# Performance work log

Measured on AMD Instinct MI355X. Metric: run time of the kernel, lower is better.

Reference implementation:

```python
import jax, jax.numpy as jnp
import numpy as np

L, H, DK = 4, 8, 64
NEG = -1e9
PAD = -9999.0


def _ln(z, g, b, eps=1e-6):
    # LayerNormalization: uses unbiased std (torch default) and divides by (std + eps)
    m = jnp.mean(z, axis=-1, keepdims=True)
    s = jnp.std(z, axis=-1, keepdims=True, ddof=1)
    return g * (z - m) / (s + eps) + b


def _mha(q_in, kv_in, w, bw, pw, pb, lnp, mask):
    B, Sq, D = q_in.shape
    q = (q_in @ w[0] + bw[0]).reshape(B, Sq, H, DK).transpose(0, 2, 1, 3)
    k = (kv_in @ w[1] + bw[1]).reshape(B, -1, H, DK).transpose(0, 2, 1, 3)
    v = (kv_in @ w[2] + bw[2]).reshape(B, -1, H, DK).transpose(0, 2, 1, 3)
    scores = jnp.einsum('bhqd,bhkd->bhqk', q, k) * (1.0 / np.sqrt(DK))
    if mask is not None:
        scores = jnp.where(mask[:, None, :, :], NEG, scores)
    attn = jax.nn.softmax(scores, axis=-1)
    ctx = jnp.einsum('bhqk,bhkd->bhqd', attn, v).transpose(0, 2, 1, 3).reshape(B, Sq, H * DK)
    return _ln(q_in + ctx @ pw + pb, lnp[0], lnp[1])


def _ffn(x, w1, b1, w2, b2, lnp):
    # kernel-1 conv1d == pointwise linear; w1:[d_ff,d_model], w2:[d_model,d_ff]
    h = jax.nn.relu(jnp.einsum('bsd,fd->bsf', x, w1) + b1)
    o = jnp.einsum('bsf,df->bsd', h, w2) + b2
    return _ln(x + o, lnp[0], lnp[1])


def _forward(enc_inputs, dec_inputs, emb_w, emb_b, pos_table,
             e_qkv_w, e_qkv_b, e_pw, e_pb, e_ln1, e_w1, e_b1, e_w2, e_b2, e_ln2,
             ds_qkv_w, ds_qkv_b, ds_pw, ds_pb, d_ln1,
             dc_qkv_w, dc_qkv_b, dc_pw, dc_pb, d_ln2,
             d_w1, d_b1, d_w2, d_b2, d_ln3):
    B, Se, F = enc_inputs.shape
    Sd = dec_inputs.shape[1]
    # ConvEmbeddingLayer: kernel-1 conv producing (d_model - n_features) channels, concat with raw inputs
    enc = jnp.concatenate([enc_inputs, jnp.einsum('bsf,of->bso', enc_inputs, emb_w) + emb_b], axis=-1)
    dec = jnp.concatenate([dec_inputs, jnp.einsum('bsf,of->bso', dec_inputs, emb_w) + emb_b], axis=-1)
    # PosEncoding with full lengths -> rows 1..S of the padded table
    enc = enc + pos_table[1:Se + 1]
    dec = dec + pos_table[1:Sd + 1]
    # masks per get_attn_pad_mask / get_attn_subsequent_mask
    enc_pad = jnp.sum(enc_inputs, axis=-1) <= PAD  # [B,Se]
    dec_pad = jnp.sum(dec_inputs, axis=-1) <= PAD  # [B,Sd]
    enc_mask = jnp.broadcast_to(enc_pad[:, None, :], (B, Se, Se))
    causal = jnp.triu(jnp.ones((Sd, Sd), dtype=bool), 1)
    dec_self_mask = jnp.broadcast_to(dec_pad[:, None, :], (B, Sd, Sd)) | causal
    cross_mask = jnp.broadcast_to(enc_pad[:, None, :], (B, Sd, Se))
    for i in range(L):
        enc = _mha(enc, enc, e_qkv_w[i], e_qkv_b[i], e_pw[i], e_pb[i], e_ln1[i], enc_mask)
        enc = _ffn(enc, e_w1[i], e_b1[i], e_w2[i], e_b2[i], e_ln2[i])
    for i in range(L):
        dec = _mha(dec, dec, ds_qkv_w[i], ds_qkv_b[i], ds_pw[i], ds_pb[i], d_ln1[i], dec_self_mask)
        dec = _mha(dec, enc, dc_qkv_w[i], dc_qkv_b[i], dc_pw[i], dc_pb[i], d_ln2[i], cross_mask)
        dec = _ffn(dec, d_w1[i], d_b1[i], d_w2[i], d_b2[i], d_ln3[i])
    return dec


def setup_inputs() -> dict:
    B, Se, Sd, F, Dm, Dff = 8, 512, 512, 32, 512, 2048
    key = jax.random.key(0)
    ks = iter(jax.random.split(key, 32))
    s = 0.02

    def n(shape, sc=s):
        return jax.random.normal(next(ks), shape, jnp.float32) * sc

    # sinusoidal PosEncoding table with leading pad row
    pos = np.arange(Se, dtype=np.float64)[:, None]
    j = np.arange(Dm)[None, :]
    ang = pos / np.power(10000.0, 2.0 * (j // 2) / Dm)
    ang[:, 0::2] = np.sin(ang[:, 0::2])
    ang[:, 1::2] = np.cos(ang[:, 1::2])
    pos_table = jnp.asarray(np.concatenate([np.zeros((1, Dm)), ang]).astype(np.float32))

    ln = jnp.broadcast_to(jnp.stack([jnp.ones(Dm), jnp.zeros(Dm)]), (L, 2, Dm)).astype(jnp.float32) + 0.0
    return {
        'enc_inputs': jax.random.normal(next(ks), (B, Se, F), jnp.float32),
        'dec_inputs': jax.random.normal(next(ks), (B, Sd, F), jnp.float32),
        'emb_w': n((Dm - F, F)), 'emb_b': jnp.zeros(Dm - F, jnp.float32),
        'pos_table': pos_table,
        'e_qkv_w': n((L, 3, Dm, H * DK)), 'e_qkv_b': jnp.zeros((L, 3, H * DK), jnp.float32),
        'e_pw': n((L, H * DK, Dm)), 'e_pb': jnp.zeros((L, Dm), jnp.float32), 'e_ln1': ln,
        'e_w1': n((L, Dff, Dm)), 'e_b1': jnp.zeros((L, Dff), jnp.float32),
        'e_w2': n((L, Dm, Dff)), 'e_b2': jnp.zeros((L, Dm), jnp.float32), 'e_ln2': ln,
        'ds_qkv_w': n((L, 3, Dm, H * DK)), 'ds_qkv_b': jnp.zeros((L, 3, H * DK), jnp.float32),
        'ds_pw': n((L, H * DK, Dm)), 'ds_pb': jnp.zeros((L, Dm), jnp.float32), 'd_ln1': ln,
        'dc_qkv_w': n((L, 3, Dm, H * DK)), 'dc_qkv_b': jnp.zeros((L, 3, H * DK), jnp.float32),
        'dc_pw': n((L, H * DK, Dm)), 'dc_pb': jnp.zeros((L, Dm), jnp.float32), 'd_ln2': ln,
        'd_w1': n((L, Dff, Dm)), 'd_b1': jnp.zeros((L, Dff), jnp.float32),
        'd_w2': n((L, Dm, Dff)), 'd_b2': jnp.zeros((L, Dm), jnp.float32), 'd_ln3': ln,
    }


def reference(enc_inputs, dec_inputs, emb_w, emb_b, pos_table,
              e_qkv_w, e_qkv_b, e_pw, e_pb, e_ln1, e_w1, e_b1, e_w2, e_b2, e_ln2,
              ds_qkv_w, ds_qkv_b, ds_pw, ds_pb, d_ln1,
              dc_qkv_w, dc_qkv_b, dc_pw, dc_pb, d_ln2,
              d_w1, d_b1, d_w2, d_b2, d_ln3):
    return _forward(enc_inputs, dec_inputs, emb_w, emb_b, pos_table,
                    e_qkv_w, e_qkv_b, e_pw, e_pb, e_ln1, e_w1, e_b1, e_w2, e_b2, e_ln2,
                    ds_qkv_w, ds_qkv_b, ds_pw, ds_pb, d_ln1,
                    dc_qkv_w, dc_qkv_b, dc_pw, dc_pb, d_ln2,
                    d_w1, d_b1, d_w2, d_b2, d_ln3)
```

## Files before the change

kernel.cpp:

```cpp
#include <hip/hip_runtime.h>
#include <cstdint>
#include <cstddef>

typedef unsigned short u16;
typedef __bf16 bf16x8 __attribute__((ext_vector_type(8)));
typedef float f32x4 __attribute__((ext_vector_type(4)));

constexpr int Bz = 8, Sq = 512, Hh = 8, DKd = 64, Dm = 512, Dff = 2048, NL = 4;
constexpr int TOK = Bz * Sq;
constexpr size_t MAT = (size_t)512 * 512;
constexpr size_t EL  = (size_t)TOK * Dm;
constexpr size_t WFT = (size_t)Dff * Dm;

__device__ __forceinline__ float bf2f(u16 u) {
  union { uint32_t i; float f; } v; v.i = (uint32_t)u << 16; return v.f;
}
__device__ __forceinline__ u16 f2bf(float f) {
  union { float f; uint32_t i; } v; v.f = f;
  uint32_t i = v.i;
  i += 0x7fffu + ((i >> 16) & 1u);
  return (u16)(i >> 16);
}

__device__ __forceinline__ void gload16(const u16* g, u16* l) {
  __builtin_amdgcn_global_load_lds(
      (const __attribute__((address_space(1))) unsigned int*)g,
      (__attribute__((address_space(3))) unsigned int*)l, 16, 0, 0);
}

template<int BM, int BN>
__global__ __launch_bounds__(256)
void gemm_tile(const u16* __restrict__ A, const u16* __restrict__ Bt,
               const float* __restrict__ bias, u16* __restrict__ C,
               int K, int lda, long long sA, int ldb, long long sB,
               int ldc, long long sC, int cmode, int relu, int colofs,
               const u16* A2, int xsplit)
{
  constexpr int HM = BM / 2, HN = BN / 2, MI = HM / 16, NI = HN / 16;
  __shared__ __align__(16) u16 As[BM * 64];
  __shared__ __align__(16) u16 Bs[BN * 64];
  const int bz = blockIdx.z;
  const u16* Abase = A;
  int colbase;
  if (A2 && (int)blockIdx.x >= xsplit) {
    Abase = A2;
    colbase = 512 + ((int)blockIdx.x - xsplit) * BN;
  } else {
    colbase = colofs + (int)blockIdx.x * BN;
  }
  const u16* Ab = Abase + (size_t)bz * (size_t)sA + (size_t)(blockIdx.y * BM) * lda;
  const u16* Bb = Bt + (size_t)bz * (size_t)sB + (size_t)colbase * ldb;
  const int tid  = threadIdx.x;
  const int lane = tid & 63;
  const int wid  = tid >> 6;
  const int l15  = lane & 15;
  const int quad = lane >> 4;
  const int wm   = wid >> 1, wn = wid & 1;

  f32x4 acc[MI][NI] = {};

  for (int k0 = 0; k0 < K; k0 += 64) {
#pragma unroll
    for (int i = 0; i < BM / 32; ++i) {
      const int s = tid + i * 256;
      const int row = s >> 3, c = (s & 7) ^ (row & 7);
      gload16(Ab + (size_t)row * lda + k0 + c * 8, As + s * 8);
    }
#pragma unroll
    for (int i = 0; i < BN / 32; ++i) {
      const int s = tid + i * 256;
      const int row = s >> 3, c = (s & 7) ^ (row & 7);
      gload16(Bb + (size_t)row * ldb + k0 + c * 8, Bs + s * 8);
    }
    __syncthreads();
#pragma unroll
    for (int kk = 0; kk < 2; ++kk) {
      bf16x8 af[MI], bfr[NI];
#pragma unroll
      for (int mi = 0; mi < MI; ++mi) {
        const int ra = wm * HM + mi * 16 + l15;
        af[mi] = *(const bf16x8*)(As + ra * 64 + (((kk * 4 + quad) ^ (ra & 7))) * 8);
      }
#pragma unroll
      for (int ni = 0; ni < NI; ++ni) {
        const int rb = wn * HN + ni * 16 + l15;
        bfr[ni] = *(const bf16x8*)(Bs + rb * 64 + (((kk * 4 + quad) ^ (rb & 7))) * 8);
      }
#pragma unroll
      for (int mi = 0; mi < MI; ++mi)
#pragma unroll
        for (int ni = 0; ni < NI; ++ni)
          acc[mi][ni] = __builtin_amdgcn_mfma_f32_16x16x32_bf16(af[mi], bfr[ni], acc[mi][ni], 0, 0, 0);
    }
    __syncthreads();
  }

  const int rblk = blockIdx.y * BM + wm * HM + quad * 4;
#pragma unroll
  for (int ni = 0; ni < NI; ++ni) {
    const int colx = colbase + wn * HN + ni * 16 + l15;
    const float bv = bias ? bias[colx] : 0.f;
#pragma unroll
    for (int mi = 0; mi < MI; ++mi) {
#pragma unroll
      for (int r = 0; r < 4; ++r) {
        float v = acc[mi][ni][r] + bv;
        if (relu) v = fmaxf(v, 0.f);
        const int grow = rblk + mi * 16 + r;
        size_t off;
        if (cmode == 0) {
          off = (size_t)bz * (size_t)sC + (size_t)grow * ldc + colx;
        } else {
          const int sec = colx >> 9, n = colx & 511, h = n >> 6, d = n & 63;
          const int b = grow >> 9, s = grow & 511;
          if (sec == 0) v *= 0.125f;
          if (sec < 2) off = (size_t)sec * EL + (size_t)b * 262144 + (size_t)h * 32768 + (size_t)s * 64 + d;
          else         off = 2 * EL + (size_t)b * 262144 + (size_t)h * 32768 + (size_t)d * 512 + s;
        }
        C[off] = f2bf(v);
      }
    }
  }
}

__global__ __launch_bounds__(256)
void flash_attn(const u16* __restrict__ q, const u16* __restrict__ k,
                const u16* __restrict__ v, const unsigned char* __restrict__ pad,
                u16* __restrict__ ctx, int mtype)
{
  __shared__ __align__(16) u16 KVs[8192];
  __shared__ __align__(16) u16 Pw[4][2048];
  const int bh = blockIdx.y, b = bh >> 3, h = bh & 7;
  const int qt = blockIdx.x;
  const int tid = threadIdx.x, lane = tid & 63, wid = tid >> 6;
  const int l15 = lane & 15, quad = lane >> 4;
  const size_t bho = (size_t)bh * 32768;
  const int qrow = qt * 64 + wid * 16 + l15;
  const int qcd  = qt * 64 + wid * 16 + quad * 4;

  unsigned char* Ps = (unsigned char*)&Pw[0][0];
  if (tid < 128) ((uchar4*)Ps)[tid] = ((const uchar4*)(pad + b * 512))[tid];

  bf16x8 aq0 = *(const bf16x8*)(q + bho + (size_t)qrow * 64 + quad * 8);
  bf16x8 aq1 = *(const bf16x8*)(q + bho + (size_t)qrow * 64 + 32 + quad * 8);

  f32x4 S[32];
#pragma unroll
  for (int kc = 0; kc < 4; ++kc) {
    __syncthreads();
#pragma unroll
    for (int i = 0; i < 4; ++i) {
      const int s = tid + i * 256;
      const int row = s >> 3, c = (s & 7) ^ (row & 7);
      gload16(k + bho + (size_t)(kc * 128 + row) * 64 + c * 8, KVs + s * 8);
    }
    __syncthreads();
#pragma unroll
    for (int t = 0; t < 8; ++t) {
      const int sw = l15 & 7;
      bf16x8 b0 = *(const bf16x8*)(KVs + (t * 16 + l15) * 64 + (quad ^ sw) * 8);
      bf16x8 b1 = *(const bf16x8*)(KVs + (t * 16 + l15) * 64 + ((4 + quad) ^ sw) * 8);
      f32x4 z = {0.f, 0.f, 0.f, 0.f};
      z = __builtin_amdgcn_mfma_f32_16x16x32_bf16(aq0, b0, z, 0, 0, 0);
      S[kc * 8 + t] = __builtin_amdgcn_mfma_f32_16x16x32_bf16(aq1, b1, z, 0, 0, 0);
    }
  }

  unsigned pm = 0u;
#pragma unroll
  for (int t = 0; t < 32; ++t) pm |= (unsigned)(Ps[t * 16 + l15] != 0) << t;

  float inv[4];
#pragma unroll
  for (int r = 0; r < 4; ++r) {
    const int qg = qcd + r;
    float mx = -3.0e38f;
#pragma unroll
    for (int t = 0; t < 32; ++t) {
      const int col = t * 16 + l15;
      const bool m = ((pm >> t) & 1u) || (mtype == 1 && col > qg);
      const float val = m ? -1e9f : S[t][r];
      S[t][r] = val;
      mx = fmaxf(mx, val);
    }
#pragma unroll
    for (int o = 8; o > 0; o >>= 1) mx = fmaxf(mx, __shfl_xor(mx, o));
    float sm = 0.f;
#pragma unroll
    for (int t = 0; t < 32; ++t) { const float e = __expf(S[t][r] - mx); S[t][r] = e; sm += e; }
#pragma unroll
    for (int o = 8; o > 0; o >>= 1) sm += __shfl_xor(sm, o);
    inv[r] = 1.f / sm;
  }

  f32x4 O[4] = {};
  u16* myP = &Pw[wid][0];
#pragma unroll
  for (int kc = 0; kc < 4; ++kc) {
    __syncthreads();
#pragma unroll
    for (int i = 0; i < 4; ++i) {
      const int s = tid + i * 256;
      const int row = s >> 4, c = (s & 15) ^ (row & 15);
      gload16(v + bho + (size_t)row * 512 + kc * 128 + c * 8, KVs + s * 8);
    }
#pragma unroll
    for (int t = 0; t < 8; ++t)
#pragma unroll
      for (int r = 0; r < 4; ++r) {
        const int rowq = quad * 4 + r;
        const int c = 2 * t + (l15 >> 3);
        myP[rowq * 128 + (c ^ rowq) * 8 + (l15 & 7)] = f2bf(S[kc * 8 + t][r] * inv[r]);
      }
    __syncthreads();
#pragma unroll
    for (int kk = 0; kk < 4; ++kk) {
      bf16x8 ap = *(const bf16x8*)(myP + l15 * 128 + ((kk * 4 + quad) ^ l15) * 8);
#pragma unroll
      for (int ni = 0; ni < 4; ++ni) {
        bf16x8 bv = *(const bf16x8*)(KVs + (ni * 16 + l15) * 128 + ((kk * 4 + quad) ^ l15) * 8);
        O[ni] = __builtin_amdgcn_mfma_f32_16x16x32_bf16(ap, bv, O[ni], 0, 0, 0);
      }
    }
  }

  const int token = b * 512 + qcd;
#pragma unroll
  for (int ni = 0; ni < 4; ++ni)
#pragma unroll
    for (int r = 0; r < 4; ++r)
      ctx[(size_t)(token + r) * 512 + h * 64 + ni * 16 + l15] = f2bf(O[ni][r]);
}

__global__ __launch_bounds__(256)
void transpose_all(const float* __restrict__ s0, const float* __restrict__ s1,
                   const float* __restrict__ s2, const float* __restrict__ s3,
                   const float* __restrict__ s4, const float* __restrict__ s5,
                   u16* __restrict__ out)
{
  __shared__ float tile[32][33];
  const int z = blockIdx.z;
  const float* src; int zi;
  if      (z < 12) { src = s0; zi = z; }
  else if (z < 24) { src = s1; zi = z - 12; }
  else if (z < 36) { src = s2; zi = z - 24; }
  else if (z < 40) { src = s3; zi = z - 36; }
  else if (z < 44) { src = s4; zi = z - 40; }
  else             { src = s5; zi = z - 44; }
  const float* in = src + (size_t)zi * MAT;
  u16* o = out + (size_t)z * MAT;
  int x = blockIdx.x * 32 + threadIdx.x;
  int y = blockIdx.y * 32 + threadIdx.y;
#pragma unroll
  for (int i = 0; i < 32; i += 8)
    tile[threadIdx.y + i][threadIdx.x] = in[(size_t)(y + i) * 512 + x];
  __syncthreads();
  x = blockIdx.y * 32 + threadIdx.x;
  y = blockIdx.x * 32 + threadIdx.y;
#pragma unroll
  for (int i = 0; i < 32; i += 8)
    o[(size_t)(y + i) * 512 + x] = f2bf(tile[threadIdx.x][threadIdx.y + i]);
}

__global__ __launch_bounds__(256)
void convert4(const float* __restrict__ a, const float* __restrict__ b,
              const float* __restrict__ c, const float* __restrict__ d,
              u16* __restrict__ out, int n)
{
  const float* srcs[4] = { a, b, c, d };
  const float* src = srcs[blockIdx.y];
  u16* dst = out + (size_t)blockIdx.y * n;
  int i = (blockIdx.x * 256 + threadIdx.x) * 4;
  if (i < n) {
    float4 v = *(const float4*)(src + i);
    ushort4 u = { f2bf(v.x), f2bf(v.y), f2bf(v.z), f2bf(v.w) };
    *(ushort4*)(dst + i) = u;
  }
}

__global__ __launch_bounds__(256)
void embed_k(const float* __restrict__ x, const float* __restrict__ ew,
             const float* __restrict__ eb, const float* __restrict__ pos,
             u16* __restrict__ out, unsigned char* __restrict__ padv)
{
  const int rs = blockIdx.x;
  const int s  = rs & 511;
  __shared__ float xr[32];
  const int t = threadIdx.x;
  if (t < 32) xr[t] = x[(size_t)rs * 32 + t];
  __syncthreads();
  if (t == 0) {
    float sacc = 0.f;
#pragma unroll
    for (int f = 0; f < 32; ++f) sacc += xr[f];
    padv[rs] = (sacc <= -9999.f) ? 1 : 0;
  }
#pragma unroll
  for (int rep = 0; rep < 2; ++rep) {
    const int c = t + rep * 256;
    float v;
    if (c < 32) {
      v = xr[c];
    } else {
      const float* w = ew + (size_t)(c - 32) * 32;
      float acc = eb[c - 32];
#pragma unroll
      for (int f = 0; f < 32; ++f) acc += xr[f] * w[f];
      v = acc;
    }
    v += pos[(size_t)(s + 1) * 512 + c];
    out[(size_t)rs * 512 + c] = f2bf(v);
  }
}

__global__ __launch_bounds__(256)
void add_ln(const u16* __restrict__ x, const u16* __restrict__ y,
            const float* __restrict__ g, const float* __restrict__ bb,
            u16* __restrict__ out)
{
  const int row  = blockIdx.x * 4 + (threadIdx.x >> 6);
  const int lane = threadIdx.x & 63;
  const int c0 = lane * 8;
  const size_t base = (size_t)row * Dm + c0;

  uint4 xr = *(const uint4*)(x + base);
  uint4 yr = *(const uint4*)(y + base);
  const u16* xh = (const u16*)&xr;
  const u16* yh = (const u16*)&yr;
  float z[8];
  float s = 0.f;
#pragma unroll
  for (int j = 0; j < 8; ++j) { z[j] = bf2f(xh[j]) + bf2f(yh[j]); s += z[j]; }
#pragma unroll
  for (int off = 32; off > 0; off >>= 1) s += __shfl_xor(s, off);
  const float mean = s * (1.f / 512.f);
  float ss = 0.f;
#pragma unroll
  for (int j = 0; j < 8; ++j) { z[j] -= mean; ss += z[j] * z[j]; }
#pragma unroll
  for (int off = 32; off > 0; off >>= 1) ss += __shfl_xor(ss, off);
  const float stdv = sqrtf(ss * (1.f / 511.f));
  const float inv = 1.f / (stdv + 1e-6f);

  float4 g0 = *(const float4*)(g + c0),  g1 = *(const float4*)(g + c0 + 4);
  float4 b0 = *(const float4*)(bb + c0), b1 = *(const float4*)(bb + c0 + 4);
  float gv[8] = { g0.x, g0.y, g0.z, g0.w, g1.x, g1.y, g1.z, g1.w };
  float bv[8] = { b0.x, b0.y, b0.z, b0.w, b1.x, b1.y, b1.z, b1.w };
  uint4 ow;
  u16* oh = (u16*)&ow;
#pragma unroll
  for (int j = 0; j < 8; ++j) oh[j] = f2bf(gv[j] * z[j] * inv + bv[j]);
  *(uint4*)(out + base) = ow;
}

__global__ __launch_bounds__(256)
void store_f32(const u16* __restrict__ in, float* __restrict__ out, int n)
{
  int i = (blockIdx.x * 256 + threadIdx.x) * 8;
  if (i < n) {
    uint4 raw = *(const uint4*)(in + i);
    const u16* h = (const u16*)&raw;
    float4 o0 = { bf2f(h[0]), bf2f(h[1]), bf2f(h[2]), bf2f(h[3]) };
    float4 o1 = { bf2f(h[4]), bf2f(h[5]), bf2f(h[6]), bf2f(h[7]) };
    *(float4*)(out + i) = o0;
    *(float4*)(out + i + 4) = o1;
  }
}

extern "C" void kernel_launch(void* const* d_in, const int* in_sizes, int n_in,
                              void* d_out, int out_size, void* d_ws, size_t ws_size,
                              hipStream_t stream)
{
  (void)in_sizes; (void)n_in; (void)out_size;
  const float* enc_in   = (const float*)d_in[0];
  const float* dec_in   = (const float*)d_in[1];
  const float* emb_w    = (const float*)d_in[2];
  const float* emb_b    = (const float*)d_in[3];
  const float* pos      = (const float*)d_in[4];
  const float* e_qkv_w  = (const float*)d_in[5];
  const float* e_qkv_b  = (const float*)d_in[6];
  const float* e_pw     = (const float*)d_in[7];
  const float* e_pb     = (const float*)d_in[8];
  const float* e_ln1    = (const float*)d_in[9];
  const float* e_w1     = (const float*)d_in[10];
  const float* e_b1     = (const float*)d_in[11];
  const float* e_w2     = (const float*)d_in[12];
  const float* e_b2     = (const float*)d_in[13];
  const float* e_ln2    = (const float*)d_in[14];
  const float* ds_qkv_w = (const float*)d_in[15];
  const float* ds_qkv_b = (const float*)d_in[16];
  const float* ds_pw    = (const float*)d_in[17];
  const float* ds_pb    = (const float*)d_in[18];
  const float* d_ln1    = (const float*)d_in[19];
  const float* dc_qkv_w = (const float*)d_in[20];
  const float* dc_qkv_b = (const float*)d_in[21];
  const float* dc_pw    = (const float*)d_in[22];
  const float* dc_pb    = (const float*)d_in[23];
  const float* d_ln2    = (const float*)d_in[24];
  const float* d_w1     = (const float*)d_in[25];
  const float* d_b1     = (const float*)d_in[26];
  const float* d_w2     = (const float*)d_in[27];
  const float* d_b2     = (const float*)d_in[28];
  const float* d_ln3    = (const float*)d_in[29];

  u16* ws  = (u16*)d_ws;
  u16* enc = ws;
  u16* dec = ws + EL;
  u16* qb  = ws + 2 * EL;
  u16* kb  = ws + 3 * EL;
  u16* vT  = ws + 4 * EL;
  u16* ctx = ws + 5 * EL;
  u16* t1  = ws + 6 * EL;
  u16* hff = ws + 7 * EL;
  u16* wT  = ws + 15 * EL;
  unsigned char* padE = (unsigned char*)(ws + 21 * EL);
  unsigned char* padD = padE + TOK;
  u16* wfAll = ws + 22 * EL;
  if (ws_size < 30 * EL * 2 + 2 * TOK) return;

  transpose_all<<<dim3(16, 16, 48), dim3(32, 8), 0, stream>>>(
      e_qkv_w, ds_qkv_w, dc_qkv_w, e_pw, ds_pw, dc_pw, wT);
  convert4<<<dim3(4096, 4), 256, 0, stream>>>(e_w1, e_w2, d_w1, d_w2, wfAll, (int)(4 * WFT));
  embed_k<<<TOK, 256, 0, stream>>>(enc_in, emb_w, emb_b, pos, enc, padE);
  embed_k<<<TOK, 256, 0, stream>>>(dec_in, emb_w, emb_b, pos, dec, padD);

  auto attention = [&](const u16* qsrc, const u16* kvsrc, const u16* wq3, const float* b3,
                       const u16* pwT, const float* pb, const float* ln,
                       const unsigned char* pad, int mtype, u16* x) {
    if (qsrc == kvsrc) {
      gemm_tile<64, 128><<<dim3(12, 64, 1), 256, 0, stream>>>(
          qsrc, wq3, b3, qb, 512, 512, 0, 512, 0, 0, 0, 4, 0, 0, nullptr, 0);
    } else {
      gemm_tile<64, 128><<<dim3(12, 64, 1), 256, 0, stream>>>(
          qsrc, wq3, b3, qb, 512, 512, 0, 512, 0, 0, 0, 4, 0, 0, kvsrc, 4);
    }
    flash_attn<<<dim3(8, 64), 256, 0, stream>>>(qb, kb, vT, pad, ctx, mtype);
    gemm_tile<64, 64><<<dim3(8, 64, 1), 256, 0, stream>>>(
        ctx, pwT, pb, t1, 512, 512, 0, 512, 0, 512, 0, 0, 0, 0, nullptr, 0);
    add_ln<<<TOK / 4, 256, 0, stream>>>(x, t1, ln, ln + 512, x);
  };

  auto ffn = [&](u16* x, const u16* w1b, const float* b1, const u16* w2b,
                 const float* b2, const float* ln) {
    gemm_tile<128, 128><<<dim3(16, 32, 1), 256, 0, stream>>>(
        x, w1b, b1, hff, 512, 512, 0, 512, 0, 2048, 0, 0, 1, 0, nullptr, 0);
    gemm_tile<64, 64><<<dim3(8, 64, 1), 256, 0, stream>>>(
        hff, w2b, b2, t1, 2048, 2048, 0, 2048, 0, 512, 0, 0, 0, 0, nullptr, 0);
    add_ln<<<TOK / 4, 256, 0, stream>>>(x, t1, ln, ln + 512, x);
  };

  for (int i = 0; i < NL; ++i) {
    attention(enc, enc, wT + (size_t)(i * 3) * MAT, e_qkv_b + i * 3 * 512,
              wT + (size_t)(36 + i) * MAT, e_pb + i * 512, e_ln1 + i * 1024, padE, 0, enc);
    ffn(enc, wfAll + (size_t)i * WFT, e_b1 + i * Dff,
        wfAll + 4 * WFT + (size_t)i * WFT, e_b2 + i * Dm, e_ln2 + i * 1024);
  }

  for (int i = 0; i < NL; ++i) {
    attention(dec, dec, wT + (size_t)(12 + i * 3) * MAT, ds_qkv_b + i * 3 * 512,
              wT + (size_t)(40 + i) * MAT, ds_pb + i * 512, d_ln1 + i * 1024, padD, 1, dec);
    attention(dec, enc, wT + (size_t)(24 + i * 3) * MAT, dc_qkv_b + i * 3 * 512,
              wT + (size_t)(44 + i) * MAT, dc_pb + i * 512, d_ln2 + i * 1024, padE, 2, dec);
    ffn(dec, wfAll + 8 * WFT + (size_t)i * WFT, d_b1 + i * Dff,
        wfAll + 12 * WFT + (size_t)i * WFT, d_b2 + i * Dm, d_ln3 + i * 1024);
  }

  store_f32<<<(int)(EL / 8 / 256), 256, 0, stream>>>(dec, (float*)d_out, (int)EL);
}
```

Baseline: 1.301 ms.

## Deepen GEMM K-tile to 128, shrink FFN1 tile, merge prep kernels and fuse final store

The GEMM template gains a BK parameter and every GEMM now stages 128-wide K slices in LDS, with an extended XOR swizzle. This halves the number of barrier-separated iterations at the cost of larger LDS use per block. The FFN up-projection moves from 128x128 to 64x128 tiles to launch more blocks. Separately, the weight transpose and convert kernels are merged into one launch, the two embedding launches into one, and the final fp32 store is folded into the last layernorm, which removes launches and one pass over the output.

```diff
diff --git a/kernel.cpp b/kernel.cpp
--- a/kernel.cpp
+++ b/kernel.cpp
@@ -28,7 +28,7 @@
       (__attribute__((address_space(3))) unsigned int*)l, 16, 0, 0);
 }
 
-template<int BM, int BN>
+template<int BM, int BN, int BK>
 __global__ __launch_bounds__(256)
 void gemm_tile(const u16* __restrict__ A, const u16* __restrict__ Bt,
                const float* __restrict__ bias, u16* __restrict__ C,
@@ -37,8 +37,9 @@
                const u16* A2, int xsplit)
 {
   constexpr int HM = BM / 2, HN = BN / 2, MI = HM / 16, NI = HN / 16;
-  __shared__ __align__(16) u16 As[BM * 64];
-  __shared__ __align__(16) u16 Bs[BN * 64];
+  constexpr int CPR = BK / 8;
+  __shared__ __align__(16) u16 As[BM * BK];
+  __shared__ __align__(16) u16 Bs[BN * BK];
   const int bz = blockIdx.z;
   const u16* Abase = A;
   int colbase;
@@ -59,32 +60,38 @@
 
   f32x4 acc[MI][NI] = {};
 
-  for (int k0 = 0; k0 < K; k0 += 64) {
-#pragma unroll
-    for (int i = 0; i < BM / 32; ++i) {
+  for (int k0 = 0; k0 < K; k0 += BK) {
+#pragma unroll
+    for (int i = 0; i < (BM * CPR) / 256; ++i) {
       const int s = tid + i * 256;
-      const int row = s >> 3, c = (s & 7) ^ (row & 7);
+      const int row = s / CPR, cl = s % CPR;
+      const int c = (cl & 8) | ((cl ^ row) & 7);
       gload16(Ab + (size_t)row * lda + k0 + c * 8, As + s * 8);
     }
 #pragma unroll
-    for (int i = 0; i < BN / 32; ++i) {
+    for (int i = 0; i < (BN * CPR) / 256; ++i) {
       const int s = tid + i * 256;
-      const int row = s >> 3, c = (s & 7) ^ (row & 7);
+      const int row = s / CPR, cl = s % CPR;
+      const int c = (cl & 8) | ((cl ^ row) & 7);
       gload16(Bb + (size_t)row * ldb + k0 + c * 8, Bs + s * 8);
     }
     __syncthreads();
 #pragma unroll
-    for (int kk = 0; kk < 2; ++kk) {
+    for (int kk = 0; kk < BK / 32; ++kk) {
       bf16x8 af[MI], bfr[NI];
 #pragma unroll
       for (int mi = 0; mi < MI; ++mi) {
         const int ra = wm * HM + mi * 16 + l15;
-        af[mi] = *(const bf16x8*)(As + ra * 64 + (((kk * 4 + quad) ^ (ra & 7))) * 8);
+        const int ch = kk * 4 + quad;
+        const int sw = (ch & 8) | ((ch ^ ra) & 7);
+        af[mi] = *(const bf16x8*)(As + ra * BK + sw * 8);
       }
 #pragma unroll
       for (int ni = 0; ni < NI; ++ni) {
         const int rb = wn * HN + ni * 16 + l15;
-        bfr[ni] = *(const bf16x8*)(Bs + rb * 64 + (((kk * 4 + quad) ^ (rb & 7))) * 8);
+        const int ch = kk * 4 + quad;
+        const int sw = (ch & 8) | ((ch ^ rb) & 7);
+        bfr[ni] = *(const bf16x8*)(Bs + rb * BK + sw * 8);
       }
 #pragma unroll
       for (int mi = 0; mi < MI; ++mi)
@@ -233,45 +240,45 @@
 }
 
 __global__ __launch_bounds__(256)
-void transpose_all(const float* __restrict__ s0, const float* __restrict__ s1,
-                   const float* __restrict__ s2, const float* __restrict__ s3,
-                   const float* __restrict__ s4, const float* __restrict__ s5,
-                   u16* __restrict__ out)
+void prep_weights(const float* __restrict__ s0, const float* __restrict__ s1,
+                  const float* __restrict__ s2, const float* __restrict__ s3,
+                  const float* __restrict__ s4, const float* __restrict__ s5,
+                  u16* __restrict__ outT,
+                  const float* __restrict__ c0, const float* __restrict__ c1,
+                  const float* __restrict__ c2, const float* __restrict__ c3,
+                  u16* __restrict__ outC)
 {
   __shared__ float tile[32][33];
   const int z = blockIdx.z;
-  const float* src; int zi;
-  if      (z < 12) { src = s0; zi = z; }
-  else if (z < 24) { src = s1; zi = z - 12; }
-  else if (z < 36) { src = s2; zi = z - 24; }
-  else if (z < 40) { src = s3; zi = z - 36; }
-  else if (z < 44) { src = s4; zi = z - 40; }
-  else             { src = s5; zi = z - 44; }
-  const float* in = src + (size_t)zi * MAT;
-  u16* o = out + (size_t)z * MAT;
-  int x = blockIdx.x * 32 + threadIdx.x;
-  int y = blockIdx.y * 32 + threadIdx.y;
-#pragma unroll
-  for (int i = 0; i < 32; i += 8)
-    tile[threadIdx.y + i][threadIdx.x] = in[(size_t)(y + i) * 512 + x];
-  __syncthreads();
-  x = blockIdx.y * 32 + threadIdx.x;
-  y = blockIdx.x * 32 + threadIdx.y;
-#pragma unroll
-  for (int i = 0; i < 32; i += 8)
-    o[(size_t)(y + i) * 512 + x] = f2bf(tile[threadIdx.x][threadIdx.y + i]);
-}
-
-__global__ __launch_bounds__(256)
-void convert4(const float* __restrict__ a, const float* __restrict__ b,
-              const float* __restrict__ c, const float* __restrict__ d,
-              u16* __restrict__ out, int n)
-{
-  const float* srcs[4] = { a, b, c, d };
-  const float* src = srcs[blockIdx.y];
-  u16* dst = out + (size_t)blockIdx.y * n;
-  int i = (blockIdx.x * 256 + threadIdx.x) * 4;
-  if (i < n) {
+  if (z < 48) {
+    const float* src; int zi;
+    if      (z < 12) { src = s0; zi = z; }
+    else if (z < 24) { src = s1; zi = z - 12; }
+    else if (z < 36) { src = s2; zi = z - 24; }
+    else if (z < 40) { src = s3; zi = z - 36; }
+    else if (z < 44) { src = s4; zi = z - 40; }
+    else             { src = s5; zi = z - 44; }
+    const float* in = src + (size_t)zi * MAT;
+    u16* o = outT + (size_t)z * MAT;
+    int x = blockIdx.x * 32 + threadIdx.x;
+    int y = blockIdx.y * 32 + threadIdx.y;
+#pragma unroll
+    for (int i = 0; i < 32; i += 8)
+      tile[threadIdx.y + i][threadIdx.x] = in[(size_t)(y + i) * 512 + x];
+    __syncthreads();
+    x = blockIdx.y * 32 + threadIdx.x;
+    y = blockIdx.x * 32 + threadIdx.y;
+#pragma unroll
+    for (int i = 0; i < 32; i += 8)
+      o[(size_t)(y + i) * 512 + x] = f2bf(tile[threadIdx.x][threadIdx.y + i]);
+  } else {
+    const int tid = threadIdx.y * 32 + threadIdx.x;
+    const int L = (z - 48) * 256 + blockIdx.y * 16 + blockIdx.x;
+    const int tens = L >> 12, bx = L & 4095;
+    const float* srcs[4] = { c0, c1, c2, c3 };
+    const float* src = srcs[tens];
+    u16* dst = outC + (size_t)tens * (4 * WFT);
+    const int i = (bx * 256 + tid) * 4;
     float4 v = *(const float4*)(src + i);
     ushort4 u = { f2bf(v.x), f2bf(v.y), f2bf(v.z), f2bf(v.w) };
     *(ushort4*)(dst + i) = u;
@@ -279,10 +286,15 @@
 }
 
 __global__ __launch_bounds__(256)
-void embed_k(const float* __restrict__ x, const float* __restrict__ ew,
-             const float* __restrict__ eb, const float* __restrict__ pos,
-             u16* __restrict__ out, unsigned char* __restrict__ padv)
-{
+void embed2(const float* __restrict__ xe, const float* __restrict__ xd,
+            const float* __restrict__ ew, const float* __restrict__ eb,
+            const float* __restrict__ pos,
+            u16* __restrict__ oute, u16* __restrict__ outd,
+            unsigned char* __restrict__ pe, unsigned char* __restrict__ pd)
+{
+  const float* x = blockIdx.y ? xd : xe;
+  u16* out = blockIdx.y ? outd : oute;
+  unsigned char* padv = blockIdx.y ? pd : pe;
   const int rs = blockIdx.x;
   const int s  = rs & 511;
   __shared__ float xr[32];
@@ -316,7 +328,7 @@
 __global__ __launch_bounds__(256)
 void add_ln(const u16* __restrict__ x, const u16* __restrict__ y,
             const float* __restrict__ g, const float* __restrict__ bb,
-            u16* __restrict__ out)
+            u16* __restrict__ out, float* __restrict__ out32)
 {
   const int row  = blockIdx.x * 4 + (threadIdx.x >> 6);
   const int lane = threadIdx.x & 63;
@@ -346,24 +358,20 @@
   float4 b0 = *(const float4*)(bb + c0), b1 = *(const float4*)(bb + c0 + 4);
   float gv[8] = { g0.x, g0.y, g0.z, g0.w, g1.x, g1.y, g1.z, g1.w };
   float bv[8] = { b0.x, b0.y, b0.z, b0.w, b1.x, b1.y, b1.z, b1.w };
-  uint4 ow;
-  u16* oh = (u16*)&ow;
-#pragma unroll
-  for (int j = 0; j < 8; ++j) oh[j] = f2bf(gv[j] * z[j] * inv + bv[j]);
-  *(uint4*)(out + base) = ow;
-}
-
-__global__ __launch_bounds__(256)
-void store_f32(const u16* __restrict__ in, float* __restrict__ out, int n)
-{
-  int i = (blockIdx.x * 256 + threadIdx.x) * 8;
-  if (i < n) {
-    uint4 raw = *(const uint4*)(in + i);
-    const u16* h = (const u16*)&raw;
-    float4 o0 = { bf2f(h[0]), bf2f(h[1]), bf2f(h[2]), bf2f(h[3]) };
-    float4 o1 = { bf2f(h[4]), bf2f(h[5]), bf2f(h[6]), bf2f(h[7]) };
-    *(float4*)(out + i) = o0;
-    *(float4*)(out + i + 4) = o1;
+  float o[8];
+#pragma unroll
+  for (int j = 0; j < 8; ++j) o[j] = gv[j] * z[j] * inv + bv[j];
+  if (out32) {
+    float4 w0 = { o[0], o[1], o[2], o[3] };
+    float4 w1 = { o[4], o[5], o[6], o[7] };
+    *(float4*)(out32 + base) = w0;
+    *(float4*)(out32 + base + 4) = w1;
+  } else {
+    uint4 ow;
+    u16* oh = (u16*)&ow;
+#pragma unroll
+    for (int j = 0; j < 8; ++j) oh[j] = f2bf(o[j]);
+    *(uint4*)(out + base) = ow;
   }
 }
 
@@ -418,42 +426,42 @@
   u16* wfAll = ws + 22 * EL;
   if (ws_size < 30 * EL * 2 + 2 * TOK) return;
 
-  transpose_all<<<dim3(16, 16, 48), dim3(32, 8), 0, stream>>>(
-      e_qkv_w, ds_qkv_w, dc_qkv_w, e_pw, ds_pw, dc_pw, wT);
-  convert4<<<dim3(4096, 4), 256, 0, stream>>>(e_w1, e_w2, d_w1, d_w2, wfAll, (int)(4 * WFT));
-  embed_k<<<TOK, 256, 0, stream>>>(enc_in, emb_w, emb_b, pos, enc, padE);
-  embed_k<<<TOK, 256, 0, stream>>>(dec_in, emb_w, emb_b, pos, dec, padD);
+  prep_weights<<<dim3(16, 16, 112), dim3(32, 8), 0, stream>>>(
+      e_qkv_w, ds_qkv_w, dc_qkv_w, e_pw, ds_pw, dc_pw, wT,
+      e_w1, e_w2, d_w1, d_w2, wfAll);
+  embed2<<<dim3(TOK, 2), 256, 0, stream>>>(enc_in, dec_in, emb_w, emb_b, pos,
+                                           enc, dec, padE, padD);
 
   auto attention = [&](const u16* qsrc, const u16* kvsrc, const u16* wq3, const float* b3,
                        const u16* pwT, const float* pb, const float* ln,
                        const unsigned char* pad, int mtype, u16* x) {
     if (qsrc == kvsrc) {
-      gemm_tile<64, 128><<<dim3(12, 64, 1), 256, 0, stream>>>(
+      gemm_tile<64, 128, 128><<<dim3(12, 64, 1), 256, 0, stream>>>(
           qsrc, wq3, b3, qb, 512, 512, 0, 512, 0, 0, 0, 4, 0, 0, nullptr, 0);
     } else {
-      gemm_tile<64, 128><<<dim3(12, 64, 1), 256, 0, stream>>>(
+      gemm_tile<64, 128, 128><<<dim3(12, 64, 1), 256, 0, stream>>>(
           qsrc, wq3, b3, qb, 512, 512, 0, 512, 0, 0, 0, 4, 0, 0, kvsrc, 4);
     }
     flash_attn<<<dim3(8, 64), 256, 0, stream>>>(qb, kb, vT, pad, ctx, mtype);
-    gemm_tile<64, 64><<<dim3(8, 64, 1), 256, 0, stream>>>(
+    gemm_tile<64, 64, 128><<<dim3(8, 64, 1), 256, 0, stream>>>(
         ctx, pwT, pb, t1, 512, 512, 0, 512, 0, 512, 0, 0, 0, 0, nullptr, 0);
-    add_ln<<<TOK / 4, 256, 0, stream>>>(x, t1, ln, ln + 512, x);
+    add_ln<<<TOK / 4, 256, 0, stream>>>(x, t1, ln, ln + 512, x, nullptr);
   };
 
   auto ffn = [&](u16* x, const u16* w1b, const float* b1, const u16* w2b,
-                 const float* b2, const float* ln) {
-    gemm_tile<128, 128><<<dim3(16, 32, 1), 256, 0, stream>>>(
+                 const float* b2, const float* ln, float* o32) {
+    gemm_tile<64, 128, 128><<<dim3(16, 64, 1), 256, 0, stream>>>(
         x, w1b, b1, hff, 512, 512, 0, 512, 0, 2048, 0, 0, 1, 0, nullptr, 0);
-    gemm_tile<64, 64><<<dim3(8, 64, 1), 256, 0, stream>>>(
+    gemm_tile<64, 64, 128><<<dim3(8, 64, 1), 256, 0, stream>>>(
         hff, w2b, b2, t1, 2048, 2048, 0, 2048, 0, 512, 0, 0, 0, 0, nullptr, 0);
-    add_ln<<<TOK / 4, 256, 0, stream>>>(x, t1, ln, ln + 512, x);
+    add_ln<<<TOK / 4, 256, 0, stream>>>(x, t1, ln, ln + 512, x, o32);
   };
 
   for (int i = 0; i < NL; ++i) {
     attention(enc, enc, wT + (size_t)(i * 3) * MAT, e_qkv_b + i * 3 * 512,
               wT + (size_t)(36 + i) * MAT, e_pb + i * 512, e_ln1 + i * 1024, padE, 0, enc);
     ffn(enc, wfAll + (size_t)i * WFT, e_b1 + i * Dff,
-        wfAll + 4 * WFT + (size_t)i * WFT, e_b2 + i * Dm, e_ln2 + i * 1024);
+        wfAll + 4 * WFT + (size_t)i * WFT, e_b2 + i * Dm, e_ln2 + i * 1024, nullptr);
   }
 
   for (int i = 0; i < NL; ++i) {
@@ -462,8 +470,7 @@
     attention(dec, enc, wT + (size_t)(24 + i * 3) * MAT, dc_qkv_b + i * 3 * 512,
               wT + (size_t)(44 + i) * MAT, dc_pb + i * 512, d_ln2 + i * 1024, padE, 2, dec);
     ffn(dec, wfAll + 8 * WFT + (size_t)i * WFT, d_b1 + i * Dff,
-        wfAll + 12 * WFT + (size_t)i * WFT, d_b2 + i * Dm, d_ln3 + i * 1024);
-  }
-
-  store_f32<<<(int)(EL / 8 / 256), 256, 0, stream>>>(dec, (float*)d_out, (int)EL);
-}
+        wfAll + 12 * WFT + (size_t)i * WFT, d_b2 + i * Dm, d_ln3 + i * 1024,
+        (i == NL - 1) ? (float*)d_out : nullptr);
+  }
+}
```

Result: no change. 1.311 ms (+0.7%).
